# Kernel tuning notes

Hardware: AMD Instinct MI355X
Metric: run time of the kernel (lower is better)

## Reference

```python
import jax, jax.numpy as jnp
import numpy as np

N = 50000
E = 800000
D = 128
H = 6


def _feast(x, src, dst, W, u, c, b, n):
    # x: [N, D]; W: [H, D_out, D_in]; u: [H, D]; c: [H]; b: [D_out]
    xj = x[src]                                  # [E, D] gathered source features
    xi = x[dst]                                  # [E, D]
    q = jax.nn.softmax((xj - xi) @ u.T + c, axis=1)   # [E, H], softmax over heads
    deg = jnp.clip(jax.ops.segment_sum(jnp.ones(src.shape[0], x.dtype), dst, num_segments=n), 1.0)
    out = jnp.broadcast_to(b, (n, b.shape[0]))
    for h in range(W.shape[0]):  # small fixed head loop avoids [E,H,D] intermediate
        agg = jax.ops.segment_sum(xj * q[:, h:h + 1], dst, num_segments=n)  # [N, D]
        out = out + (agg / deg[:, None]) @ W[h].T
    return out


def setup_inputs() -> dict:
    key = jax.random.key(0)
    ks = jax.random.split(key, 32)
    s = 0.05
    inp = {
        'pos': jax.random.normal(ks[0], (N, 3), jnp.float32),
        'norm': jax.random.normal(ks[1], (N, 3), jnp.float32),
        'edge_index': jax.random.randint(ks[2], (2, E), 0, N, jnp.int32),
        'w1': jax.random.normal(ks[3], (D, 6), jnp.float32) * s,
        'b1': jnp.zeros((D,), jnp.float32),
        'w2': jax.random.normal(ks[4], (3, D), jnp.float32) * s,
        'b2': jnp.zeros((3,), jnp.float32),
    }
    for l in range(4):
        inp[f'Wg{l+1}'] = jax.random.normal(ks[5 + 4 * l], (H, D, D), jnp.float32) * s
        inp[f'u{l+1}'] = jax.random.normal(ks[6 + 4 * l], (H, D), jnp.float32) * s
        inp[f'c{l+1}'] = jnp.zeros((H,), jnp.float32)
        inp[f'bg{l+1}'] = jnp.zeros((D,), jnp.float32)
    return inp


def reference(pos, norm, edge_index, w1, b1, w2, b2,
              Wg1, u1, c1, bg1, Wg2, u2, c2, bg2,
              Wg3, u3, c3, bg3, Wg4, u4, c4, bg4):
    src, dst = edge_index[0], edge_index[1]
    n = pos.shape[0]
    x = jnp.concatenate([pos, norm], axis=1)          # [N, 6]
    x = jax.nn.relu(x @ w1.T + b1)                    # conv1d_1 (kernel=1) == linear
    for (Wg, u, c, bg) in ((Wg1, u1, c1, bg1), (Wg2, u2, c2, bg2),
                           (Wg3, u3, c3, bg3), (Wg4, u4, c4, bg4)):
        x = jax.nn.relu(_feast(x, src, dst, Wg, u, c, bg, n))  # dropout identity at eval
    return x @ w2.T + b2                              # conv1d_2 (kernel=1) == linear -> [N, 3]
```

## Files before the change

### kernel.cpp

```cpp
#include <hip/hip_runtime.h>
#include <hip/hip_fp16.h>

#define DD 128
#define HH 6

typedef _Float16 f16;
typedef _Float16 f16x2 __attribute__((ext_vector_type(2)));
typedef _Float16 f16x8 __attribute__((ext_vector_type(8)));
typedef float f32x4 __attribute__((ext_vector_type(4)));

__global__ void enc_kernel(const float* __restrict__ pos, const float* __restrict__ nrm,
                           const float* __restrict__ w1, const float* __restrict__ b1,
                           f16* __restrict__ x, int n) {
  int i = blockIdx.x;
  int d = threadIdx.x;
  if (i >= n) return;
  float in[6];
  in[0] = pos[i*3+0]; in[1] = pos[i*3+1]; in[2] = pos[i*3+2];
  in[3] = nrm[i*3+0]; in[4] = nrm[i*3+1]; in[5] = nrm[i*3+2];
  const float* wr = w1 + d*6;
  float acc = b1[d];
  #pragma unroll
  for (int k = 0; k < 6; k++) acc = fmaf(in[k], wr[k], acc);
  x[(size_t)i*DD + d] = (f16)fmaxf(acc, 0.0f);
}

__global__ void hist_kernel(const int* __restrict__ dst, int e, int* __restrict__ cnt) {
  int i = blockIdx.x*blockDim.x + threadIdx.x;
  if (i < e) atomicAdd(&cnt[dst[i]], 1);
}

__global__ void scan_blk_kernel(const int* __restrict__ cnt, int* __restrict__ rowptr,
                                int* __restrict__ bsum, int n) {
  __shared__ int s[256];
  int tid = threadIdx.x;
  int i = blockIdx.x*256 + tid;
  int v = (i < n) ? cnt[i] : 0;
  s[tid] = v; __syncthreads();
  #pragma unroll
  for (int off = 1; off < 256; off <<= 1) {
    int t = (tid >= off) ? s[tid-off] : 0;
    __syncthreads();
    s[tid] += t;
    __syncthreads();
  }
  if (i < n) rowptr[i] = s[tid] - v;
  if (tid == 255) bsum[blockIdx.x] = s[255];
}

__global__ void scan_top_kernel(int* bsum, int nb) {
  __shared__ int s[256];
  int tid = threadIdx.x;
  int v = (tid < nb) ? bsum[tid] : 0;
  s[tid] = v; __syncthreads();
  #pragma unroll
  for (int off = 1; off < 256; off <<= 1) {
    int t = (tid >= off) ? s[tid-off] : 0;
    __syncthreads();
    s[tid] += t;
    __syncthreads();
  }
  if (tid < nb) bsum[tid] = s[tid] - v;
}

__global__ void scan_add_kernel(int* rowptr, const int* __restrict__ bsum,
                                const int* __restrict__ cnt, float* __restrict__ invdeg,
                                int n, int e) {
  int i = blockIdx.x*256 + threadIdx.x;
  if (i < n) {
    rowptr[i] += bsum[blockIdx.x];
    invdeg[i] = 1.0f / (float)max(cnt[i], 1);
  }
  if (i == 0) rowptr[n] = e;
}

__global__ void fill_kernel(const int* __restrict__ src, const int* __restrict__ dst, int e,
                            const int* __restrict__ rowptr, int* __restrict__ fc,
                            int2* __restrict__ sd_pair) {
  int i = blockIdx.x*blockDim.x + threadIdx.x;
  if (i >= e) return;
  int dd = dst[i];
  int p = rowptr[dd] + atomicAdd(&fc[dd], 1);
  sd_pair[p] = make_int2(src[i], dd);
}

__global__ void z_kernel(const f16* __restrict__ x, const float* __restrict__ u,
                         float* __restrict__ z, int n) {
  int node = blockIdx.x*4 + (threadIdx.x >> 6);
  int l = threadIdx.x & 63;
  if (node >= n) return;
  f16x2 v = *(const f16x2*)&x[(size_t)node*DD + 2*l];
  float vx = (float)v[0], vy = (float)v[1];
  float p[HH];
  #pragma unroll
  for (int h = 0; h < HH; h++) {
    float2 uv = *(const float2*)&u[h*DD + 2*l];
    p[h] = vx*uv.x + vy*uv.y;
  }
  #pragma unroll
  for (int off = 32; off; off >>= 1) {
    #pragma unroll
    for (int h = 0; h < HH; h++) p[h] += __shfl_xor(p[h], off, 64);
  }
  if (l == 0) {
    #pragma unroll
    for (int h = 0; h < HH; h++) z[(size_t)node*HH + h] = p[h];
  }
}

__global__ void q_kernel(const int2* __restrict__ sd_pair,
                         const float* __restrict__ z, const float* __restrict__ c,
                         const float* __restrict__ invdeg,
                         f16* __restrict__ qcsr, int e) {
  int i = blockIdx.x*blockDim.x + threadIdx.x;
  if (i >= e) return;
  int2 sd = sd_pair[i];
  int s = sd.x, dd = sd.y;
  float l[HH];
  float m = -1e30f;
  #pragma unroll
  for (int h = 0; h < HH; h++) {
    l[h] = z[(size_t)s*HH + h] - z[(size_t)dd*HH + h] + c[h];
    m = fmaxf(m, l[h]);
  }
  float sum = 0.f;
  #pragma unroll
  for (int h = 0; h < HH; h++) { l[h] = __expf(l[h] - m); sum += l[h]; }
  float r = invdeg[dd] / sum;
  size_t p = (size_t)i*HH;
  f16x2 o0 = {(f16)(l[0]*r), (f16)(l[1]*r)};
  f16x2 o1 = {(f16)(l[2]*r), (f16)(l[3]*r)};
  f16x2 o2 = {(f16)(l[4]*r), (f16)(l[5]*r)};
  *(f16x2*)&qcsr[p+0] = o0;
  *(f16x2*)&qcsr[p+2] = o1;
  *(f16x2*)&qcsr[p+4] = o2;
}

__global__ __launch_bounds__(256) void agg_kernel(const f16* __restrict__ x,
                           const f16* __restrict__ qcsr,
                           const int* __restrict__ rowptr, const int2* __restrict__ sd_pair,
                           f16* __restrict__ agg, int n) {
  int node = blockIdx.x*4 + (threadIdx.x >> 6);
  int t = threadIdx.x & 63;
  if (node >= n) return;
  float acc0[HH] = {0,0,0,0,0,0};
  float acc1[HH] = {0,0,0,0,0,0};
  int p0 = rowptr[node], p1 = rowptr[node+1];
  int p = p0;
  for (; p + 4 <= p1; p += 4) {
    int s[4];
    #pragma unroll
    for (int u = 0; u < 4; u++) s[u] = sd_pair[p+u].x;
    f16x2 xv[4];
    #pragma unroll
    for (int u = 0; u < 4; u++) xv[u] = *(const f16x2*)&x[(size_t)s[u]*DD + 2*t];
    const f16x2* qp = (const f16x2*)(qcsr + (size_t)p*HH);
    f16x2 qv[12];
    #pragma unroll
    for (int u = 0; u < 12; u++) qv[u] = qp[u];
    #pragma unroll
    for (int u = 0; u < 4; u++) {
      float x0 = (float)xv[u][0], x1 = (float)xv[u][1];
      float qh[HH] = {(float)qv[u*3+0][0], (float)qv[u*3+0][1],
                      (float)qv[u*3+1][0], (float)qv[u*3+1][1],
                      (float)qv[u*3+2][0], (float)qv[u*3+2][1]};
      #pragma unroll
      for (int h = 0; h < HH; h++) {
        acc0[h] = fmaf(qh[h], x0, acc0[h]);
        acc1[h] = fmaf(qh[h], x1, acc1[h]);
      }
    }
  }
  for (; p < p1; p++) {
    int s = sd_pair[p].x;
    const f16x2* qp = (const f16x2*)(qcsr + (size_t)p*HH);
    f16x2 q01 = qp[0], q23 = qp[1], q45 = qp[2];
    f16x2 xv = *(const f16x2*)&x[(size_t)s*DD + 2*t];
    float x0 = (float)xv[0], x1 = (float)xv[1];
    float qh[HH] = {(float)q01[0], (float)q01[1], (float)q23[0],
                    (float)q23[1], (float)q45[0], (float)q45[1]};
    #pragma unroll
    for (int h = 0; h < HH; h++) {
      acc0[h] = fmaf(qh[h], x0, acc0[h]);
      acc1[h] = fmaf(qh[h], x1, acc1[h]);
    }
  }
  #pragma unroll
  for (int h = 0; h < HH; h++) {
    f16x2 o = {(f16)acc0[h], (f16)acc1[h]};
    __builtin_nontemporal_store(__builtin_bit_cast(unsigned, o),
        (unsigned*)&agg[(size_t)node*768 + h*DD + 2*t]);
  }
}

__global__ void wc4_kernel(const float* __restrict__ W0, const float* __restrict__ W1,
                           const float* __restrict__ W2, const float* __restrict__ W3,
                           f16* __restrict__ Wc) {
  int id = blockIdx.x*256 + threadIdx.x;
  if (id >= 4*HH*DD*DD) return;
  int l = id / (HH*DD*DD);
  int r = id - l*(HH*DD*DD);
  const float* W = (l == 0) ? W0 : (l == 1) ? W1 : (l == 2) ? W2 : W3;
  int h = r >> 14, rem = r & 16383, nr = rem >> 7, d = rem & 127;
  Wc[(size_t)l*(HH*DD*DD) + (size_t)nr*768 + h*DD + d] = (f16)W[r];
}

__global__ __launch_bounds__(256) void gemm_kernel(const f16* __restrict__ A,
                                                   const f16* __restrict__ Wc,
                                                   const float* __restrict__ bias,
                                                   f16* __restrict__ xout, int n) {
  __shared__ char lds[65536];
  const int t = threadIdx.x;
  const int l = t & 63;
  const int wave = t >> 6;
  const int wr = wave >> 1, wc = wave & 1;
  const int r16 = l & 15, kc = l >> 4;
  const int m0 = blockIdx.x * 128;

  const int sr0 = t >> 3;
  const int scb = (t & 7) * 16;

  auto stage = [&](int ks, int buf) {
    const int k0 = ks * 64;
    char* Ad = lds + buf * 16384 + (size_t)t * 16;
    char* Bd = lds + 32768 + buf * 16384 + (size_t)t * 16;
    #pragma unroll
    for (int i = 0; i < 4; i++) {
      int r = i * 32 + sr0;
      int cs = (scb ^ ((r & 7) << 4)) >> 1;
      const f16* ga = A  + (size_t)(m0 + r) * 768 + k0 + cs;
      const f16* gb = Wc + (size_t)r * 768 + k0 + cs;
      __builtin_amdgcn_global_load_lds(
          (const __attribute__((address_space(1))) void*)ga,
          (__attribute__((address_space(3))) void*)(Ad + i * 4096), 16, 0, 0);
      __builtin_amdgcn_global_load_lds(
          (const __attribute__((address_space(1))) void*)gb,
          (__attribute__((address_space(3))) void*)(Bd + i * 4096), 16, 0, 0);
    }
  };

  f32x4 acc[4][4];
  #pragma unroll
  for (int m = 0; m < 4; m++)
    #pragma unroll
    for (int nn = 0; nn < 4; nn++) acc[m][nn] = (f32x4){0.f, 0.f, 0.f, 0.f};

  stage(0, 0);
  __syncthreads();

  const int xr = (r16 & 7) << 4;
  for (int ks = 0; ks < 12; ks++) {
    int buf = ks & 1;
    if (ks < 11) stage(ks + 1, buf ^ 1);
    const char* Ab = lds + buf * 16384;
    const char* Bb = lds + 32768 + buf * 16384;
    #pragma unroll
    for (int kk = 0; kk < 2; kk++) {
      int kb = (kk * 64 + kc * 16) ^ xr;
      f16x8 a[4], b[4];
      #pragma unroll
      for (int m = 0; m < 4; m++)
        a[m] = *(const f16x8*)(Ab + (wr*64 + m*16 + r16) * 128 + kb);
      #pragma unroll
      for (int nn = 0; nn < 4; nn++)
        b[nn] = *(const f16x8*)(Bb + (wc*64 + nn*16 + r16) * 128 + kb);
      #pragma unroll
      for (int m = 0; m < 4; m++)
        #pragma unroll
        for (int nn = 0; nn < 4; nn++)
          acc[m][nn] = __builtin_amdgcn_mfma_f32_16x16x32_f16(a[m], b[nn], acc[m][nn], 0, 0, 0);
    }
    __syncthreads();
  }

  #pragma unroll
  for (int nn = 0; nn < 4; nn++) {
    int col = wc*64 + nn*16 + r16;
    float bv = bias[col];
    #pragma unroll
    for (int m = 0; m < 4; m++) {
      int rbase = m0 + wr*64 + m*16 + kc*4;
      #pragma unroll
      for (int rr = 0; rr < 4; rr++) {
        int gm = rbase + rr;
        if (gm < n) xout[(size_t)gm*DD + col] = (f16)fmaxf(acc[m][nn][rr] + bv, 0.f);
      }
    }
  }
}

__global__ void fin_kernel(const f16* __restrict__ x, const float* __restrict__ w2,
                           const float* __restrict__ b2, float* __restrict__ out, int n) {
  int node = blockIdx.x*4 + (threadIdx.x >> 6);
  int l = threadIdx.x & 63;
  if (node >= n) return;
  f16x2 v = *(const f16x2*)&x[(size_t)node*DD + 2*l];
  float vx = (float)v[0], vy = (float)v[1];
  float p[3];
  #pragma unroll
  for (int o = 0; o < 3; o++) {
    float2 w = *(const float2*)&w2[o*DD + 2*l];
    p[o] = vx*w.x + vy*w.y;
  }
  #pragma unroll
  for (int off = 32; off; off >>= 1) {
    #pragma unroll
    for (int o = 0; o < 3; o++) p[o] += __shfl_xor(p[o], off, 64);
  }
  if (l == 0) {
    #pragma unroll
    for (int o = 0; o < 3; o++) out[(size_t)node*3 + o] = p[o] + b2[o];
  }
}

extern "C" void kernel_launch(void* const* d_in, const int* in_sizes, int n_in,
                              void* d_out, int out_size, void* d_ws, size_t ws_size,
                              hipStream_t stream) {
  const float* pos = (const float*)d_in[0];
  const float* nrm = (const float*)d_in[1];
  const int*   ei  = (const int*)d_in[2];
  const float* w1  = (const float*)d_in[3];
  const float* b1  = (const float*)d_in[4];
  const float* w2  = (const float*)d_in[5];
  const float* b2  = (const float*)d_in[6];
  const float* Wg[4] = {(const float*)d_in[7],  (const float*)d_in[11],
                        (const float*)d_in[15], (const float*)d_in[19]};
  const float* uu[4] = {(const float*)d_in[8],  (const float*)d_in[12],
                        (const float*)d_in[16], (const float*)d_in[20]};
  const float* cc[4] = {(const float*)d_in[9],  (const float*)d_in[13],
                        (const float*)d_in[17], (const float*)d_in[21]};
  const float* bg[4] = {(const float*)d_in[10], (const float*)d_in[14],
                        (const float*)d_in[18], (const float*)d_in[22]};
  int n = in_sizes[0] / 3;
  int e = in_sizes[2] / 2;
  const int* src = ei;
  const int* dst = ei + e;

  char* p = (char*)d_ws;
  auto alloc = [&](size_t bytes) -> void* {
    void* r = (void*)p;
    p += (bytes + 255) & ~(size_t)255;
    return r;
  };
  f16*   xa     = (f16*)alloc((size_t)n*DD*2);
  f16*   xb     = (f16*)alloc((size_t)n*DD*2);
  f16*   agg    = (f16*)alloc((size_t)n*768*2 + 131072);
  f16*   qcsr   = (f16*)alloc((size_t)e*HH*2);
  f16*   wcb    = (f16*)alloc((size_t)4*HH*DD*DD*2);
  float* zbuf   = (float*)alloc((size_t)n*HH*4);
  float* invdeg = (float*)alloc((size_t)n*4);
  int*   cnt    = (int*)alloc((size_t)n*4);
  int*   rowptr = (int*)alloc((size_t)(n+1)*4);
  int*   fc     = (int*)alloc((size_t)n*4);
  int2*  sd_pair= (int2*)alloc((size_t)e*8);
  int*   bsum   = (int*)alloc(4096);

  hipMemsetAsync(cnt, 0, (size_t)n*4, stream);
  hipMemsetAsync(fc,  0, (size_t)n*4, stream);

  int eb = (e + 255)/256;
  int nb = (n + 255)/256;

  enc_kernel<<<n, 128, 0, stream>>>(pos, nrm, w1, b1, xa, n);
  hist_kernel<<<eb, 256, 0, stream>>>(dst, e, cnt);
  wc4_kernel<<<(4*HH*DD*DD + 255)/256, 256, 0, stream>>>(Wg[0], Wg[1], Wg[2], Wg[3], wcb);
  scan_blk_kernel<<<nb, 256, 0, stream>>>(cnt, rowptr, bsum, n);
  scan_top_kernel<<<1, 256, 0, stream>>>(bsum, nb);
  scan_add_kernel<<<nb, 256, 0, stream>>>(rowptr, bsum, cnt, invdeg, n, e);
  fill_kernel<<<eb, 256, 0, stream>>>(src, dst, e, rowptr, fc, sd_pair);

  f16* xin = xa;
  f16* xout = xb;
  for (int l = 0; l < 4; l++) {
    z_kernel<<<(n+3)/4, 256, 0, stream>>>(xin, uu[l], zbuf, n);
    q_kernel<<<eb, 256, 0, stream>>>(sd_pair, zbuf, cc[l], invdeg, qcsr, e);
    agg_kernel<<<(n+3)/4, 256, 0, stream>>>(xin, qcsr, rowptr, sd_pair, agg, n);
    gemm_kernel<<<(n+127)/128, 256, 0, stream>>>(agg, wcb + (size_t)l*HH*DD*DD, bg[l], xout, n);
    f16* t = xin; xin = xout; xout = t;
  }
  fin_kernel<<<(n+3)/4, 256, 0, stream>>>(xin, w2, b2, (float*)d_out, n);
}
```

Before: 625.1 us.

## Fuse per-head aggregation into the GEMM via LDS-resident A tile

Merges the aggregation kernel and the weight GEMM into one kernel. Each 512-thread block aggregates 32 nodes into a swizzled LDS A-tile and then multiplies it by double-buffered weight tiles with MFMA. This drops the round trip of the [N,768] fp16 aggregation buffer through global memory and one launch per layer. In exchange, each block now re-streams the whole weight matrix for only 32 rows instead of 128, uses 80 KB of LDS which limits occupancy, and waits on the irregular gather before the MFMA phase can start.

```diff
diff --git a/kernel.cpp b/kernel.cpp
--- a/kernel.cpp
+++ b/kernel.cpp
@@ -136,63 +136,6 @@
   *(f16x2*)&qcsr[p+4] = o2;
 }
 
-__global__ __launch_bounds__(256) void agg_kernel(const f16* __restrict__ x,
-                           const f16* __restrict__ qcsr,
-                           const int* __restrict__ rowptr, const int2* __restrict__ sd_pair,
-                           f16* __restrict__ agg, int n) {
-  int node = blockIdx.x*4 + (threadIdx.x >> 6);
-  int t = threadIdx.x & 63;
-  if (node >= n) return;
-  float acc0[HH] = {0,0,0,0,0,0};
-  float acc1[HH] = {0,0,0,0,0,0};
-  int p0 = rowptr[node], p1 = rowptr[node+1];
-  int p = p0;
-  for (; p + 4 <= p1; p += 4) {
-    int s[4];
-    #pragma unroll
-    for (int u = 0; u < 4; u++) s[u] = sd_pair[p+u].x;
-    f16x2 xv[4];
-    #pragma unroll
-    for (int u = 0; u < 4; u++) xv[u] = *(const f16x2*)&x[(size_t)s[u]*DD + 2*t];
-    const f16x2* qp = (const f16x2*)(qcsr + (size_t)p*HH);
-    f16x2 qv[12];
-    #pragma unroll
-    for (int u = 0; u < 12; u++) qv[u] = qp[u];
-    #pragma unroll
-    for (int u = 0; u < 4; u++) {
-      float x0 = (float)xv[u][0], x1 = (float)xv[u][1];
-      float qh[HH] = {(float)qv[u*3+0][0], (float)qv[u*3+0][1],
-                      (float)qv[u*3+1][0], (float)qv[u*3+1][1],
-                      (float)qv[u*3+2][0], (float)qv[u*3+2][1]};
-      #pragma unroll
-      for (int h = 0; h < HH; h++) {
-        acc0[h] = fmaf(qh[h], x0, acc0[h]);
-        acc1[h] = fmaf(qh[h], x1, acc1[h]);
-      }
-    }
-  }
-  for (; p < p1; p++) {
-    int s = sd_pair[p].x;
-    const f16x2* qp = (const f16x2*)(qcsr + (size_t)p*HH);
-    f16x2 q01 = qp[0], q23 = qp[1], q45 = qp[2];
-    f16x2 xv = *(const f16x2*)&x[(size_t)s*DD + 2*t];
-    float x0 = (float)xv[0], x1 = (float)xv[1];
-    float qh[HH] = {(float)q01[0], (float)q01[1], (float)q23[0],
-                    (float)q23[1], (float)q45[0], (float)q45[1]};
-    #pragma unroll
-    for (int h = 0; h < HH; h++) {
-      acc0[h] = fmaf(qh[h], x0, acc0[h]);
-      acc1[h] = fmaf(qh[h], x1, acc1[h]);
-    }
-  }
-  #pragma unroll
-  for (int h = 0; h < HH; h++) {
-    f16x2 o = {(f16)acc0[h], (f16)acc1[h]};
-    __builtin_nontemporal_store(__builtin_bit_cast(unsigned, o),
-        (unsigned*)&agg[(size_t)node*768 + h*DD + 2*t]);
-  }
-}
-
 __global__ void wc4_kernel(const float* __restrict__ W0, const float* __restrict__ W1,
                            const float* __restrict__ W2, const float* __restrict__ W3,
                            f16* __restrict__ Wc) {
@@ -205,86 +148,126 @@
   Wc[(size_t)l*(HH*DD*DD) + (size_t)nr*768 + h*DD + d] = (f16)W[r];
 }
 
-__global__ __launch_bounds__(256) void gemm_kernel(const f16* __restrict__ A,
-                                                   const f16* __restrict__ Wc,
-                                                   const float* __restrict__ bias,
-                                                   f16* __restrict__ xout, int n) {
-  __shared__ char lds[65536];
+__global__ __launch_bounds__(512) void fused_kernel(const f16* __restrict__ x,
+                           const f16* __restrict__ qcsr,
+                           const int* __restrict__ rowptr, const int2* __restrict__ sd_pair,
+                           const f16* __restrict__ Wc, const float* __restrict__ bias,
+                           f16* __restrict__ xout, int n) {
+  __shared__ char lds[81920];
   const int t = threadIdx.x;
   const int l = t & 63;
   const int wave = t >> 6;
-  const int wr = wave >> 1, wc = wave & 1;
-  const int r16 = l & 15, kc = l >> 4;
-  const int m0 = blockIdx.x * 128;
-
-  const int sr0 = t >> 3;
-  const int scb = (t & 7) * 16;
-
-  auto stage = [&](int ks, int buf) {
-    const int k0 = ks * 64;
-    char* Ad = lds + buf * 16384 + (size_t)t * 16;
-    char* Bd = lds + 32768 + buf * 16384 + (size_t)t * 16;
-    #pragma unroll
-    for (int i = 0; i < 4; i++) {
-      int r = i * 32 + sr0;
-      int cs = (scb ^ ((r & 7) << 4)) >> 1;
-      const f16* ga = A  + (size_t)(m0 + r) * 768 + k0 + cs;
-      const f16* gb = Wc + (size_t)r * 768 + k0 + cs;
-      __builtin_amdgcn_global_load_lds(
-          (const __attribute__((address_space(1))) void*)ga,
-          (__attribute__((address_space(3))) void*)(Ad + i * 4096), 16, 0, 0);
+  const int tile = blockIdx.x * 32;
+
+  for (int i = 0; i < 4; i++) {
+    int nl = wave * 4 + i;
+    int node = tile + nl;
+    float acc0[HH] = {0,0,0,0,0,0};
+    float acc1[HH] = {0,0,0,0,0,0};
+    if (node < n) {
+      int p0 = rowptr[node], p1 = rowptr[node+1];
+      int p = p0;
+      for (; p + 4 <= p1; p += 4) {
+        int s[4];
+        #pragma unroll
+        for (int u = 0; u < 4; u++) s[u] = sd_pair[p+u].x;
+        f16x2 xv[4];
+        #pragma unroll
+        for (int u = 0; u < 4; u++) xv[u] = *(const f16x2*)&x[(size_t)s[u]*DD + 2*l];
+        const f16x2* qp = (const f16x2*)(qcsr + (size_t)p*HH);
+        f16x2 qv[12];
+        #pragma unroll
+        for (int u = 0; u < 12; u++) qv[u] = qp[u];
+        #pragma unroll
+        for (int u = 0; u < 4; u++) {
+          float x0 = (float)xv[u][0], x1 = (float)xv[u][1];
+          float qh[HH] = {(float)qv[u*3+0][0], (float)qv[u*3+0][1],
+                          (float)qv[u*3+1][0], (float)qv[u*3+1][1],
+                          (float)qv[u*3+2][0], (float)qv[u*3+2][1]};
+          #pragma unroll
+          for (int h = 0; h < HH; h++) {
+            acc0[h] = fmaf(qh[h], x0, acc0[h]);
+            acc1[h] = fmaf(qh[h], x1, acc1[h]);
+          }
+        }
+      }
+      for (; p < p1; p++) {
+        int s = sd_pair[p].x;
+        const f16x2* qp = (const f16x2*)(qcsr + (size_t)p*HH);
+        f16x2 q01 = qp[0], q23 = qp[1], q45 = qp[2];
+        f16x2 xv = *(const f16x2*)&x[(size_t)s*DD + 2*l];
+        float x0 = (float)xv[0], x1 = (float)xv[1];
+        float qh[HH] = {(float)q01[0], (float)q01[1], (float)q23[0],
+                        (float)q23[1], (float)q45[0], (float)q45[1]};
+        #pragma unroll
+        for (int h = 0; h < HH; h++) {
+          acc0[h] = fmaf(qh[h], x0, acc0[h]);
+          acc1[h] = fmaf(qh[h], x1, acc1[h]);
+        }
+      }
+    }
+    char* Arow = lds + nl * 1536;
+    int swz = (nl & 7) << 4;
+    #pragma unroll
+    for (int h = 0; h < HH; h++) {
+      f16x2 o = {(f16)acc0[h], (f16)acc1[h]};
+      *(f16x2*)(Arow + ((h*256 + 4*l) ^ swz)) = o;
+    }
+  }
+
+  auto stageB = [&](int ks, int buf) {
+    int k0 = ks * 64;
+    char* Bd = lds + 49152 + buf * 16384 + t * 16;
+    #pragma unroll
+    for (int i = 0; i < 2; i++) {
+      int r = (t >> 3) + i * 64;
+      int cb = ((t & 7) * 16) ^ ((r & 7) << 4);
+      const f16* gb = Wc + (size_t)r * 768 + k0 + (cb >> 1);
       __builtin_amdgcn_global_load_lds(
           (const __attribute__((address_space(1))) void*)gb,
-          (__attribute__((address_space(3))) void*)(Bd + i * 4096), 16, 0, 0);
+          (__attribute__((address_space(3))) void*)(Bd + i * 8192), 16, 0, 0);
     }
   };
 
-  f32x4 acc[4][4];
-  #pragma unroll
-  for (int m = 0; m < 4; m++)
-    #pragma unroll
-    for (int nn = 0; nn < 4; nn++) acc[m][nn] = (f32x4){0.f, 0.f, 0.f, 0.f};
-
-  stage(0, 0);
+  const int r16 = l & 15, kc = l >> 4;
+  const int wM = wave >> 2, wN = wave & 3;
+  const int arow = wM * 16 + r16;
+  const char* ArowB = lds + arow * 1536;
+  const int axr = (arow & 7) << 4;
+
+  f32x4 acc[2];
+  acc[0] = (f32x4){0.f,0.f,0.f,0.f};
+  acc[1] = (f32x4){0.f,0.f,0.f,0.f};
+
+  stageB(0, 0);
   __syncthreads();
 
-  const int xr = (r16 & 7) << 4;
   for (int ks = 0; ks < 12; ks++) {
     int buf = ks & 1;
-    if (ks < 11) stage(ks + 1, buf ^ 1);
-    const char* Ab = lds + buf * 16384;
-    const char* Bb = lds + 32768 + buf * 16384;
+    if (ks < 11) stageB(ks + 1, buf ^ 1);
+    const char* Bb = lds + 49152 + buf * 16384;
     #pragma unroll
     for (int kk = 0; kk < 2; kk++) {
-      int kb = (kk * 64 + kc * 16) ^ xr;
-      f16x8 a[4], b[4];
+      f16x8 a = *(const f16x8*)(ArowB + ((ks*128 + kk*64 + kc*16) ^ axr));
       #pragma unroll
-      for (int m = 0; m < 4; m++)
-        a[m] = *(const f16x8*)(Ab + (wr*64 + m*16 + r16) * 128 + kb);
-      #pragma unroll
-      for (int nn = 0; nn < 4; nn++)
-        b[nn] = *(const f16x8*)(Bb + (wc*64 + nn*16 + r16) * 128 + kb);
-      #pragma unroll
-      for (int m = 0; m < 4; m++)
-        #pragma unroll
-        for (int nn = 0; nn < 4; nn++)
-          acc[m][nn] = __builtin_amdgcn_mfma_f32_16x16x32_f16(a[m], b[nn], acc[m][nn], 0, 0, 0);
-    }
-    __syncthreads();
-  }
-
-  #pragma unroll
-  for (int nn = 0; nn < 4; nn++) {
-    int col = wc*64 + nn*16 + r16;
+      for (int nn = 0; nn < 2; nn++) {
+        int bro = wN*32 + nn*16 + r16;
+        f16x8 b = *(const f16x8*)(Bb + bro*128 + ((kk*64 + kc*16) ^ ((bro & 7) << 4)));
+        acc[nn] = __builtin_amdgcn_mfma_f32_16x16x32_f16(a, b, acc[nn], 0, 0, 0);
+      }
+    }
+    __syncthreads();
+  }
+
+  #pragma unroll
+  for (int nn = 0; nn < 2; nn++) {
+    int col = wN*32 + nn*16 + r16;
     float bv = bias[col];
-    #pragma unroll
-    for (int m = 0; m < 4; m++) {
-      int rbase = m0 + wr*64 + m*16 + kc*4;
-      #pragma unroll
-      for (int rr = 0; rr < 4; rr++) {
-        int gm = rbase + rr;
-        if (gm < n) xout[(size_t)gm*DD + col] = (f16)fmaxf(acc[m][nn][rr] + bv, 0.f);
-      }
+    int rbase = tile + wM*16 + kc*4;
+    #pragma unroll
+    for (int rr = 0; rr < 4; rr++) {
+      int gm = rbase + rr;
+      if (gm < n) xout[(size_t)gm*DD + col] = (f16)fmaxf(acc[nn][rr] + bv, 0.f);
     }
   }
 }
@@ -344,7 +327,6 @@
   };
   f16*   xa     = (f16*)alloc((size_t)n*DD*2);
   f16*   xb     = (f16*)alloc((size_t)n*DD*2);
-  f16*   agg    = (f16*)alloc((size_t)n*768*2 + 131072);
   f16*   qcsr   = (f16*)alloc((size_t)e*HH*2);
   f16*   wcb    = (f16*)alloc((size_t)4*HH*DD*DD*2);
   float* zbuf   = (float*)alloc((size_t)n*HH*4);
@@ -371,11 +353,12 @@
 
   f16* xin = xa;
   f16* xout = xb;
+  int fb = (n + 31)/32;
   for (int l = 0; l < 4; l++) {
     z_kernel<<<(n+3)/4, 256, 0, stream>>>(xin, uu[l], zbuf, n);
     q_kernel<<<eb, 256, 0, stream>>>(sd_pair, zbuf, cc[l], invdeg, qcsr, e);
-    agg_kernel<<<(n+3)/4, 256, 0, stream>>>(xin, qcsr, rowptr, sd_pair, agg, n);
-    gemm_kernel<<<(n+127)/128, 256, 0, stream>>>(agg, wcb + (size_t)l*HH*DD*DD, bg[l], xout, n);
+    fused_kernel<<<fb, 512, 0, stream>>>(xin, qcsr, rowptr, sd_pair,
+                                         wcb + (size_t)l*HH*DD*DD, bg[l], xout, n);
     f16* t = xin; xin = xout; xout = t;
   }
   fin_kernel<<<(n+3)/4, 256, 0, stream>>>(xin, w2, b2, (float*)d_out, n);
```

Result: slower. 698.6 us (+11.8%).
